# Performance work log

Hardware: AMD Instinct MI355X
Metric: run time of the kernel (lower is better)

The kernel has to match this reference:

```python
import jax, jax.numpy as jnp
import numpy as np

T, B, IN = 256, 64, 512
HIDDEN = [512, 512, 512]
DILATIONS = [1, 2, 4]


def _lstm_scan(x, W_ih, W_hh, b_ih, b_hh):
    """Run an LSTMCell over leading time axis of x: [Td, N, D] -> [Td, N, H]."""
    H = W_hh.shape[1]
    N = x.shape[1]
    h0 = jnp.zeros((N, H), x.dtype)
    c0 = jnp.zeros((N, H), x.dtype)

    def step(carry, xt):
        h, c = carry
        gates = xt @ W_ih.T + b_ih + h @ W_hh.T + b_hh  # [N, 4H], torch order i,f,g,o
        i, f, g, o = jnp.split(gates, 4, axis=-1)
        c = jax.nn.sigmoid(f) * c + jax.nn.sigmoid(i) * jnp.tanh(g)
        h = jax.nn.sigmoid(o) * jnp.tanh(c)
        return (h, c), h

    _, hs = jax.lax.scan(step, (h0, c0), x)
    return hs


def _drnn_layer(x, rate, W_ih, W_hh, b_ih, b_hh):
    """Dilated RNN layer. x: [T, B, D] with T % rate == 0.
    Torch code concats `rate` consecutive timesteps along batch -> one dilated step;
    reshape [T,B,D] -> [T//rate, rate*B, D] reproduces exactly that layout, and the
    chunk/unroll at the end is the inverse reshape."""
    Tn, Bn, D = x.shape
    Td = Tn // rate
    xd = x.reshape(Td, rate * Bn, D)
    hs = _lstm_scan(xd, W_ih, W_hh, b_ih, b_hh)  # [Td, rate*B, H]
    return hs.reshape(Tn, Bn, W_hh.shape[1])


def setup_inputs() -> dict:
    key = jax.random.key(0)
    ks = jax.random.split(key, 1 + 4 * len(HIDDEN))
    inp = {"x": jax.random.normal(ks[0], (T, B, IN), dtype=jnp.float32)}
    in_dim = IN
    ki = 1
    for li, H in enumerate(HIDDEN):
        bound = 1.0 / np.sqrt(H)
        inp[f"W_ih{li}"] = jax.random.uniform(ks[ki + 0], (4 * H, in_dim), jnp.float32, -bound, bound)
        inp[f"W_hh{li}"] = jax.random.uniform(ks[ki + 1], (4 * H, H), jnp.float32, -bound, bound)
        inp[f"b_ih{li}"] = jax.random.uniform(ks[ki + 2], (4 * H,), jnp.float32, -bound, bound)
        inp[f"b_hh{li}"] = jax.random.uniform(ks[ki + 3], (4 * H,), jnp.float32, -bound, bound)
        ki += 4
        in_dim = H
    return inp


def reference(x,
              W_ih0, W_hh0, b_ih0, b_hh0,
              W_ih1, W_hh1, b_ih1, b_hh1,
              W_ih2, W_hh2, b_ih2, b_hh2):
    params = [(W_ih0, W_hh0, b_ih0, b_hh0),
              (W_ih1, W_hh1, b_ih1, b_hh1),
              (W_ih2, W_hh2, b_ih2, b_hh2)]
    h = x
    for (Wih, Whh, bih, bhh), rate in zip(params, DILATIONS):
        h = _drnn_layer(h, rate, Wih, Whh, bih, bhh)
    return h  # [T, B, HIDDEN[-1]]
```

## Files before the change

kernel.cpp:

```cpp
#include <hip/hip_runtime.h>

typedef __attribute__((ext_vector_type(8))) short bf16x8;
typedef __attribute__((ext_vector_type(4))) float f32x4;

__device__ __forceinline__ unsigned short f2bf(float x) {
    unsigned u = __float_as_uint(x);
    u += 0x7FFFu + ((u >> 16) & 1u);
    return (unsigned short)(u >> 16);
}
__device__ __forceinline__ float sigm(float x) { return 1.0f / (1.0f + __expf(-x)); }
__device__ __forceinline__ float ftanh(float x) {
    float e = __expf(2.f * x);
    return 1.f - 2.f / (e + 1.f);
}

__device__ __forceinline__ void gld16(const unsigned short* g, unsigned short* l) {
    __builtin_amdgcn_global_load_lds((const __attribute__((address_space(1))) void*)g,
                                     (__attribute__((address_space(3))) void*)l, 16, 0, 0);
}

__device__ __forceinline__ unsigned cohload(const unsigned* p) {
    unsigned v;
    asm volatile("global_load_dword %0, %1, off sc0 sc1\n\ts_waitcnt vmcnt(0)"
                 : "=v"(v) : "v"(p) : "memory");
    return v;
}
__device__ __forceinline__ void cohstore(unsigned* p, unsigned v) {
    asm volatile("global_store_dword %0, %1, off sc0 sc1" :: "v"(p), "v"(v) : "memory");
}

__global__ __launch_bounds__(256) void k_conv_x(const float* __restrict__ x,
                                                unsigned short* __restrict__ Xp) {
    int i = blockIdx.x * 256 + threadIdx.x;
    int rb = i >> 10, kc = (i >> 6) & 15, ln = i & 63;
    int row = (rb << 4) + (ln & 15);
    int k   = (kc << 5) + ((ln >> 4) << 3);
    const float* s = x + (size_t)row * 512 + k;
    float4 v0 = *(const float4*)s, v1 = *(const float4*)(s + 4);
    unsigned short o[8] = {f2bf(v0.x), f2bf(v0.y), f2bf(v0.z), f2bf(v0.w),
                           f2bf(v1.x), f2bf(v1.y), f2bf(v1.z), f2bf(v1.w)};
    *(bf16x8*)(Xp + (size_t)i * 8) = *(bf16x8*)o;
}

__global__ __launch_bounds__(256) void k_conv_w(const float* __restrict__ Wih,
                                                const float* __restrict__ Whh,
                                                unsigned short* __restrict__ Wp) {
    int i = blockIdx.x * 256 + threadIdx.x;
    int wrb = i >> 11, kc = (i >> 6) & 31, ln = i & 63;
    int j = (wrb << 4) + (ln & 15);
    int k = (kc << 5) + ((ln >> 4) << 3);
    int srow = (j & 3) * 512 + (j >> 2);
    const float* s = (k < 512) ? (Wih + (size_t)srow * 512 + k)
                               : (Whh + (size_t)srow * 512 + (k - 512));
    float4 v0 = *(const float4*)s, v1 = *(const float4*)(s + 4);
    unsigned short o[8] = {f2bf(v0.x), f2bf(v0.y), f2bf(v0.z), f2bf(v0.w),
                           f2bf(v1.x), f2bf(v1.y), f2bf(v1.z), f2bf(v1.w)};
    *(bf16x8*)(Wp + (size_t)i * 8) = *(bf16x8*)o;
}

struct DP {
    const unsigned short* Xp;
    unsigned short *Hp0, *Hp1, *Hp2;
    const unsigned short *Wp0, *Wp1, *Wp2;
    const float *bi0, *bh0, *bi1, *bh1, *bi2, *bh2;
    float* Out;
    unsigned int* flags;
};

__device__ __forceinline__ void quadT(f32x4 a, int sq, float& G0, float& G1, float& G2, float& G3) {
    float a0 = a[0], a1 = a[1], a2 = a[2], a3 = a[3];
    float p1 = (sq & 1) ? a0 : a1; float g1_ = __shfl_xor(p1, 1);
    float p2 = (sq & 1) ? a2 : a3; float g2_ = __shfl_xor(p2, 1);
    float m0 = (sq & 1) ? g1_ : a0, m1 = (sq & 1) ? a1 : g1_;
    float m2 = (sq & 1) ? g2_ : a2, m3 = (sq & 1) ? a3 : g2_;
    float q1 = (sq & 2) ? m0 : m2; float h1_ = __shfl_xor(q1, 2);
    float q2 = (sq & 2) ? m1 : m3; float h2_ = __shfl_xor(q2, 2);
    G0 = (sq & 2) ? h1_ : m0; G1 = (sq & 2) ? h2_ : m1;
    G2 = (sq & 2) ? m2 : h1_; G3 = (sq & 2) ? m3 : h2_;
}

#define PIN8(A,B,C,D,E,F,G,H) \
    asm volatile("" : "+v"(A),"+v"(B),"+v"(C),"+v"(D),"+v"(E),"+v"(F),"+v"(G),"+v"(H))

__global__ __launch_bounds__(256, 1) void k_drnn(DP p) {
    const int tid = threadIdx.x, lane = tid & 63, wv = tid >> 6;
    const int l15 = lane & 15, lhi = lane >> 4, sq = l15 & 3;

    int b = blockIdx.x, l, c, w, T, P, N;
    if (b < 64)       { l = 0; c = b >> 5;         w = b & 31; T = 256; P = 1; N = 64; }
    else if (b < 128) { l = 1; c = (b >> 5) & 1;   w = b & 31; T = 128; P = 2; N = 128; }
    else              { l = 2; c = (b - 128) >> 5; w = b & 31; T = 64;  P = 2; N = 256; }
    const int cid = (l == 0) ? c : (l == 1 ? 2 + c : 4 + c);

    const unsigned short* Xs = (l == 0) ? p.Xp : (l == 1 ? p.Hp0 : p.Hp1);
    unsigned short*       Hd = (l == 0) ? p.Hp0 : (l == 1 ? p.Hp1 : p.Hp2);
    const unsigned short* Ws = (l == 0) ? p.Wp0 : (l == 1 ? p.Wp1 : p.Wp2);
    const float* bi = (l == 0) ? p.bi0 : (l == 1 ? p.bi1 : p.bi2);
    const float* bh = (l == 0) ? p.bh0 : (l == 1 ? p.bh1 : p.bh2);
    const int R0 = c * (P * 32);

    __shared__ unsigned short At[65536];

    const unsigned short* wbase = Ws + ((size_t)(((w << 2) + wv) * 32) << 9) + lane * 8;
#define DECLW(n) bf16x8 w##n = *(const bf16x8*)(wbase + (n << 9));
    DECLW(0) DECLW(1) DECLW(2) DECLW(3) DECLW(4) DECLW(5) DECLW(6) DECLW(7)
    DECLW(8) DECLW(9) DECLW(10) DECLW(11) DECLW(12) DECLW(13) DECLW(14) DECLW(15)
    DECLW(16) DECLW(17) DECLW(18) DECLW(19) DECLW(20) DECLW(21) DECLW(22) DECLW(23)
    DECLW(24) DECLW(25) DECLW(26) DECLW(27) DECLW(28) DECLW(29) DECLW(30) DECLW(31)

    const int hcol = (w << 4) + (wv << 2) + (l15 >> 2);
    const float bs0 = bi[hcol]        + bh[hcol];
    const float bs1 = bi[512 + hcol]  + bh[512 + hcol];
    const float bs2 = bi[1024 + hcol] + bh[1024 + hcol];
    const float bs3 = bi[1536 + hcol] + bh[1536 + hcol];

    const int kch = hcol >> 5;
    const int lane16 = (((hcol & 31) >> 3) << 4) + ((lhi << 2) + sq);
    const int st_lt = lane16 * 8 + (hcol & 7);

    float cst0 = 0.f, cst1 = 0.f, cst2 = 0.f, cst3 = 0.f;
    unsigned int* flags = p.flags;

#define KPn(na, nb) { \
    bf16x8 xa = *(const bf16x8*)(a0 + ((na) << 9)); \
    bf16x8 xb = *(const bf16x8*)(a1 + ((na) << 9)); \
    bf16x8 ya = *(const bf16x8*)(a0 + ((nb) << 9)); \
    bf16x8 yb = *(const bf16x8*)(a1 + ((nb) << 9)); \
    e0 = __builtin_amdgcn_mfma_f32_16x16x32_bf16(xa, w##na, e0, 0, 0, 0); \
    e1 = __builtin_amdgcn_mfma_f32_16x16x32_bf16(xb, w##na, e1, 0, 0, 0); \
    o0 = __builtin_amdgcn_mfma_f32_16x16x32_bf16(ya, w##nb, o0, 0, 0, 0); \
    o1 = __builtin_amdgcn_mfma_f32_16x16x32_bf16(yb, w##nb, o1, 0, 0, 0); }

#define PWST(RV, CSTV, PR) { \
    float G0, G1, G2, G3; quadT(RV, sq, G0, G1, G2, G3); \
    float cn = sigm(G1 + bs1) * CSTV + sigm(G0 + bs0) * ftanh(G2 + bs2); \
    float hn = sigm(G3 + bs3) * ftanh(cn); CSTV = cn; \
    const int Rw = RxB + (PR); \
    __hip_atomic_store(Hd + ((size_t)((Rw * 16 + kch) << 9) + st_lt), f2bf(hn), \
                       __ATOMIC_RELAXED, __HIP_MEMORY_SCOPE_AGENT); \
    if (l == 2) p.Out[((size_t)((Rw << 4) + (lhi << 2) + sq)) * 512 + hcol] = hn; }

#define DOPASS(PI, CA, CB) { \
    const unsigned short* a0 = At + (((PI) * 64) << 9) + lane * 8; \
    const unsigned short* a1 = a0 + (32 << 9); \
    f32x4 e0 = {0.f,0.f,0.f,0.f}, o0 = {0.f,0.f,0.f,0.f}; \
    f32x4 e1 = {0.f,0.f,0.f,0.f}, o1 = {0.f,0.f,0.f,0.f}; \
    KPn(0,1) KPn(2,3) KPn(4,5) KPn(6,7) KPn(8,9) KPn(10,11) KPn(12,13) KPn(14,15) \
    KPn(16,17) KPn(18,19) KPn(20,21) KPn(22,23) KPn(24,25) KPn(26,27) KPn(28,29) KPn(30,31) \
    f32x4 r0 = e0 + o0, r1 = e1 + o1; \
    PWST(r0, CA, (PI) * 2) PWST(r1, CB, (PI) * 2 + 1) }

    for (int t = 0; t < T; ++t) {
        PIN8(w0,w1,w2,w3,w4,w5,w6,w7);
        PIN8(w8,w9,w10,w11,w12,w13,w14,w15);
        PIN8(w16,w17,w18,w19,w20,w21,w22,w23);
        PIN8(w24,w25,w26,w27,w28,w29,w30,w31);

        const int RxB = (t * N + R0) >> 4;

        if (l == 0) {
            #pragma unroll
            for (int i = 0; i < 8; ++i) {
                int q = (wv << 3) + i, rb = q >> 4, kc = q & 15;
                gld16(Xs + ((size_t)((RxB + rb) * 16 + kc) << 9) + lane * 8,
                      &At[(rb * 32 + kc) << 9]);
            }
        }

        if (wv == 0 && t > 0) {
            const unsigned* fp = flags + cid * 32 + (lane & 31);
            const unsigned need = (unsigned)t;
            int n = 0;
            for (;;) {
                unsigned v = cohload(fp);
                if (__all((lane >= 32) || (v >= need))) break;
                if (++n > (1 << 20)) break;
            }
        }
        if (wv == 1 && l == 1) {
            const unsigned* fp = flags + lane;
            const unsigned need = (unsigned)(2 * t + 2);
            int n = 0;
            for (;;) {
                unsigned v = cohload(fp);
                if (__all(v >= need)) break;
                if (++n > (1 << 20)) break;
            }
        }
        if (wv == 1 && l == 2) {
            const unsigned* fp = flags + (2 + (c & 1)) * 32 + (lane & 31);
            const unsigned need = (unsigned)(2 * t + (c >> 1) + 1);
            int n = 0;
            for (;;) {
                unsigned v = cohload(fp);
                if (__all((lane >= 32) || (v >= need))) break;
                if (++n > (1 << 20)) break;
            }
        }
        __syncthreads();

        if (l == 0) {
            if (t > 0) {
                const int RhB = ((t - 1) * N + R0) >> 4;
                #pragma unroll
                for (int i = 0; i < 8; ++i) {
                    int q = (wv << 3) + i, rb = q >> 4, kc = q & 15;
                    gld16(Hd + ((size_t)((RhB + rb) * 16 + kc) << 9) + lane * 8,
                          &At[(rb * 32 + 16 + kc) << 9]);
                }
            } else {
                #pragma unroll
                for (int rb = 0; rb < 2; ++rb)
                    #pragma unroll
                    for (int it = 0; it < 4; ++it)
                        *(float4*)&At[((rb * 32 + 16) << 9) + (it * 256 + tid) * 8] =
                            (float4){0.f, 0.f, 0.f, 0.f};
            }
            __builtin_amdgcn_sched_barrier(0);

            const unsigned short* a0 = At + lane * 8;
            const unsigned short* a1 = a0 + (32 << 9);
            f32x4 e0 = {0.f,0.f,0.f,0.f}, o0 = {0.f,0.f,0.f,0.f};
            f32x4 e1 = {0.f,0.f,0.f,0.f}, o1 = {0.f,0.f,0.f,0.f};
            KPn(0,1) KPn(2,3) KPn(4,5) KPn(6,7)
            KPn(8,9) KPn(10,11) KPn(12,13) KPn(14,15)
            __syncthreads();
            KPn(16,17) KPn(18,19) KPn(20,21) KPn(22,23)
            KPn(24,25) KPn(26,27) KPn(28,29) KPn(30,31)
            f32x4 r0 = e0 + o0, r1 = e1 + o1;
            PWST(r0, cst0, 0) PWST(r1, cst1, 1)
        } else {
            #pragma unroll
            for (int i = 0; i < 16; ++i) {
                int q = (wv << 4) + i, rb = q >> 4, kc = q & 15;
                gld16(Xs + ((size_t)((RxB + rb) * 16 + kc) << 9) + lane * 8,
                      &At[(rb * 32 + kc) << 9]);
            }
            if (t > 0) {
                const int RhB = ((t - 1) * N + R0) >> 4;
                #pragma unroll
                for (int i = 0; i < 16; ++i) {
                    int q = (wv << 4) + i, rb = q >> 4, kc = q & 15;
                    gld16(Hd + ((size_t)((RhB + rb) * 16 + kc) << 9) + lane * 8,
                          &At[(rb * 32 + 16 + kc) << 9]);
                }
            } else {
                #pragma unroll
                for (int rb = 0; rb < 4; ++rb)
                    #pragma unroll
                    for (int it = 0; it < 4; ++it)
                        *(float4*)&At[((rb * 32 + 16) << 9) + (it * 256 + tid) * 8] =
                            (float4){0.f, 0.f, 0.f, 0.f};
            }
            __syncthreads();
            DOPASS(0, cst0, cst1)
            DOPASS(1, cst2, cst3)
        }

        asm volatile("s_waitcnt vmcnt(0)" ::: "memory");
        __syncthreads();
        if (tid == 0) cohstore(flags + cid * 32 + w, (unsigned)(t + 1));
    }
}

extern "C" void kernel_launch(void* const* d_in, const int* in_sizes, int n_in,
                              void* d_out, int out_size, void* d_ws, size_t ws_size,
                              hipStream_t stream)
{
    const float* x = (const float*)d_in[0];
    const float* Wih[3] = {(const float*)d_in[1], (const float*)d_in[5], (const float*)d_in[9]};
    const float* Whh[3] = {(const float*)d_in[2], (const float*)d_in[6], (const float*)d_in[10]};
    const float* bih[3] = {(const float*)d_in[3], (const float*)d_in[7], (const float*)d_in[11]};
    const float* bhh[3] = {(const float*)d_in[4], (const float*)d_in[8], (const float*)d_in[12]};

    char* wp = (char*)d_ws;
    const size_t SZ_A = (size_t)16384 * 512;
    unsigned short* Xp  = (unsigned short*)wp; wp += SZ_A * 2;
    unsigned short* Hp0 = (unsigned short*)wp; wp += SZ_A * 2;
    unsigned short* Hp1 = (unsigned short*)wp; wp += SZ_A * 2;
    unsigned short* Hp2 = (unsigned short*)wp; wp += SZ_A * 2;
    unsigned short* Wp[3];
    for (int l = 0; l < 3; ++l) { Wp[l] = (unsigned short*)wp; wp += (size_t)2048 * 1024 * 2; }
    unsigned int* flags = (unsigned int*)wp;

    hipMemsetAsync(flags, 0, 8 * 32 * sizeof(unsigned int), stream);
    k_conv_x<<<dim3(4096), dim3(256), 0, stream>>>(x, Xp);
    for (int l = 0; l < 3; ++l)
        k_conv_w<<<dim3(1024), dim3(256), 0, stream>>>(Wih[l], Whh[l], Wp[l]);

    DP dp;
    dp.Xp = Xp; dp.Hp0 = Hp0; dp.Hp1 = Hp1; dp.Hp2 = Hp2;
    dp.Wp0 = Wp[0]; dp.Wp1 = Wp[1]; dp.Wp2 = Wp[2];
    dp.bi0 = bih[0]; dp.bh0 = bhh[0];
    dp.bi1 = bih[1]; dp.bh1 = bhh[1];
    dp.bi2 = bih[2]; dp.bh2 = bhh[2];
    dp.Out = (float*)d_out; dp.flags = flags;

    k_drnn<<<dim3(256), dim3(256), 0, stream>>>(dp);
}
```

Before: 1.029 ms.

## Split intra-layer and cross-layer flags, write-through separate layer inputs, cheaper polling

The persistent wavefront kernel now keeps its recurrent hidden state in ordinary stores. It writes the next layer's input through a separate buffer with write-through (sc0 sc1) stores, and uses separate flag arrays for intra-layer and cross-layer dependencies. Intra-layer flag polling uses an L2-scope load and falls back to a system-coherent load after many spins. Blocks are interleaved across layers by blockIdx, and quad shuffles use DPP instead of ds_bpermute. The aim is to cut synchronization latency per time step, at the cost of added memory traffic and coherence assumptions about L2 visibility across XCDs.

```diff
diff --git a/kernel.cpp b/kernel.cpp
--- a/kernel.cpp
+++ b/kernel.cpp
@@ -19,14 +19,30 @@
                                      (__attribute__((address_space(3))) void*)l, 16, 0, 0);
 }
 
-__device__ __forceinline__ unsigned cohload(const unsigned* p) {
+__device__ __forceinline__ unsigned ld_l2(const unsigned* p) {
+    unsigned v;
+    asm volatile("global_load_dword %0, %1, off sc0\n\ts_waitcnt vmcnt(0)"
+                 : "=v"(v) : "v"(p) : "memory");
+    return v;
+}
+__device__ __forceinline__ unsigned ld_mall(const unsigned* p) {
     unsigned v;
     asm volatile("global_load_dword %0, %1, off sc0 sc1\n\ts_waitcnt vmcnt(0)"
                  : "=v"(v) : "v"(p) : "memory");
     return v;
 }
-__device__ __forceinline__ void cohstore(unsigned* p, unsigned v) {
+__device__ __forceinline__ void st_flag(unsigned* p, unsigned v) {
     asm volatile("global_store_dword %0, %1, off sc0 sc1" :: "v"(p), "v"(v) : "memory");
+}
+__device__ __forceinline__ void st_wt16(unsigned short* p, unsigned v) {
+    asm volatile("global_store_short %0, %1, off sc0 sc1" :: "v"(p), "v"(v) : "memory");
+}
+
+__device__ __forceinline__ float dppx1(float x) {
+    return __int_as_float(__builtin_amdgcn_mov_dpp(__float_as_int(x), 0xB1, 0xF, 0xF, true));
+}
+__device__ __forceinline__ float dppx2(float x) {
+    return __int_as_float(__builtin_amdgcn_mov_dpp(__float_as_int(x), 0x4E, 0xF, 0xF, true));
 }
 
 __global__ __launch_bounds__(256) void k_conv_x(const float* __restrict__ x,
@@ -61,6 +77,7 @@
 struct DP {
     const unsigned short* Xp;
     unsigned short *Hp0, *Hp1, *Hp2;
+    unsigned short *Xq1, *Xq2;
     const unsigned short *Wp0, *Wp1, *Wp2;
     const float *bi0, *bh0, *bi1, *bh1, *bi2, *bh2;
     float* Out;
@@ -69,12 +86,12 @@
 
 __device__ __forceinline__ void quadT(f32x4 a, int sq, float& G0, float& G1, float& G2, float& G3) {
     float a0 = a[0], a1 = a[1], a2 = a[2], a3 = a[3];
-    float p1 = (sq & 1) ? a0 : a1; float g1_ = __shfl_xor(p1, 1);
-    float p2 = (sq & 1) ? a2 : a3; float g2_ = __shfl_xor(p2, 1);
+    float p1 = (sq & 1) ? a0 : a1; float g1_ = dppx1(p1);
+    float p2 = (sq & 1) ? a2 : a3; float g2_ = dppx1(p2);
     float m0 = (sq & 1) ? g1_ : a0, m1 = (sq & 1) ? a1 : g1_;
     float m2 = (sq & 1) ? g2_ : a2, m3 = (sq & 1) ? a3 : g2_;
-    float q1 = (sq & 2) ? m0 : m2; float h1_ = __shfl_xor(q1, 2);
-    float q2 = (sq & 2) ? m1 : m3; float h2_ = __shfl_xor(q2, 2);
+    float q1 = (sq & 2) ? m0 : m2; float h1_ = dppx2(q1);
+    float q2 = (sq & 2) ? m1 : m3; float h2_ = dppx2(q2);
     G0 = (sq & 2) ? h1_ : m0; G1 = (sq & 2) ? h2_ : m1;
     G2 = (sq & 2) ? m2 : h1_; G3 = (sq & 2) ? m3 : h2_;
 }
@@ -86,14 +103,16 @@
     const int tid = threadIdx.x, lane = tid & 63, wv = tid >> 6;
     const int l15 = lane & 15, lhi = lane >> 4, sq = l15 & 3;
 
-    int b = blockIdx.x, l, c, w, T, P, N;
-    if (b < 64)       { l = 0; c = b >> 5;         w = b & 31; T = 256; P = 1; N = 64; }
-    else if (b < 128) { l = 1; c = (b >> 5) & 1;   w = b & 31; T = 128; P = 2; N = 128; }
-    else              { l = 2; c = (b - 128) >> 5; w = b & 31; T = 64;  P = 2; N = 256; }
-    const int cid = (l == 0) ? c : (l == 1 ? 2 + c : 4 + c);
-
-    const unsigned short* Xs = (l == 0) ? p.Xp : (l == 1 ? p.Hp0 : p.Hp1);
+    const int b = blockIdx.x;
+    const int cid = b & 7, w = b >> 3;
+    int l, c, T, P, N;
+    if (cid < 2)      { l = 0; c = cid;     T = 256; P = 1; N = 64;  }
+    else if (cid < 4) { l = 1; c = cid - 2; T = 128; P = 2; N = 128; }
+    else              { l = 2; c = cid - 4; T = 64;  P = 2; N = 256; }
+
+    const unsigned short* Xs = (l == 0) ? p.Xp  : (l == 1 ? p.Xq1 : p.Xq2);
     unsigned short*       Hd = (l == 0) ? p.Hp0 : (l == 1 ? p.Hp1 : p.Hp2);
+    unsigned short*       Xw = (l == 0) ? p.Xq1 : (l == 1 ? p.Xq2 : nullptr);
     const unsigned short* Ws = (l == 0) ? p.Wp0 : (l == 1 ? p.Wp1 : p.Wp2);
     const float* bi = (l == 0) ? p.bi0 : (l == 1 ? p.bi1 : p.bi2);
     const float* bh = (l == 0) ? p.bh0 : (l == 1 ? p.bh1 : p.bh2);
@@ -119,7 +138,9 @@
     const int st_lt = lane16 * 8 + (hcol & 7);
 
     float cst0 = 0.f, cst1 = 0.f, cst2 = 0.f, cst3 = 0.f;
-    unsigned int* flags = p.flags;
+    unsigned int* iflag = p.flags;
+    unsigned int* cflag = p.flags + 256;
+    int fastok = 1;
 
 #define KPn(na, nb) { \
     bf16x8 xa = *(const bf16x8*)(a0 + ((na) << 9)); \
@@ -131,16 +152,12 @@
     o0 = __builtin_amdgcn_mfma_f32_16x16x32_bf16(ya, w##nb, o0, 0, 0, 0); \
     o1 = __builtin_amdgcn_mfma_f32_16x16x32_bf16(yb, w##nb, o1, 0, 0, 0); }
 
-#define PWST(RV, CSTV, PR) { \
+#define PWC(RV, CSTV, HV) { \
     float G0, G1, G2, G3; quadT(RV, sq, G0, G1, G2, G3); \
     float cn = sigm(G1 + bs1) * CSTV + sigm(G0 + bs0) * ftanh(G2 + bs2); \
-    float hn = sigm(G3 + bs3) * ftanh(cn); CSTV = cn; \
-    const int Rw = RxB + (PR); \
-    __hip_atomic_store(Hd + ((size_t)((Rw * 16 + kch) << 9) + st_lt), f2bf(hn), \
-                       __ATOMIC_RELAXED, __HIP_MEMORY_SCOPE_AGENT); \
-    if (l == 2) p.Out[((size_t)((Rw << 4) + (lhi << 2) + sq)) * 512 + hcol] = hn; }
-
-#define DOPASS(PI, CA, CB) { \
+    HV = sigm(G3 + bs3) * ftanh(cn); CSTV = cn; }
+
+#define DOPASS(PI, CA, CB, HA, HB) { \
     const unsigned short* a0 = At + (((PI) * 64) << 9) + lane * 8; \
     const unsigned short* a1 = a0 + (32 << 9); \
     f32x4 e0 = {0.f,0.f,0.f,0.f}, o0 = {0.f,0.f,0.f,0.f}; \
@@ -148,7 +165,7 @@
     KPn(0,1) KPn(2,3) KPn(4,5) KPn(6,7) KPn(8,9) KPn(10,11) KPn(12,13) KPn(14,15) \
     KPn(16,17) KPn(18,19) KPn(20,21) KPn(22,23) KPn(24,25) KPn(26,27) KPn(28,29) KPn(30,31) \
     f32x4 r0 = e0 + o0, r1 = e1 + o1; \
-    PWST(r0, CA, (PI) * 2) PWST(r1, CB, (PI) * 2 + 1) }
+    PWC(r0, CA, HA) PWC(r1, CB, HB) }
 
     for (int t = 0; t < T; ++t) {
         PIN8(w0,w1,w2,w3,w4,w5,w6,w7);
@@ -168,37 +185,38 @@
         }
 
         if (wv == 0 && t > 0) {
-            const unsigned* fp = flags + cid * 32 + (lane & 31);
+            const unsigned* fp = iflag + cid * 32 + (lane & 31);
             const unsigned need = (unsigned)t;
             int n = 0;
             for (;;) {
-                unsigned v = cohload(fp);
+                unsigned v = fastok ? ld_l2(fp) : ld_mall(fp);
                 if (__all((lane >= 32) || (v >= need))) break;
-                if (++n > (1 << 20)) break;
+                if (fastok && ++n > 2048) fastok = 0;
             }
         }
         if (wv == 1 && l == 1) {
-            const unsigned* fp = flags + lane;
-            const unsigned need = (unsigned)(2 * t + 2);
+            const unsigned* fp = cflag + lane;
+            const unsigned need = (unsigned)(2 * t + (lane >> 5) + 1);
             int n = 0;
             for (;;) {
-                unsigned v = cohload(fp);
+                unsigned v = ld_mall(fp);
                 if (__all(v >= need)) break;
-                if (++n > (1 << 20)) break;
+                if (++n > (1 << 22)) break;
             }
         }
         if (wv == 1 && l == 2) {
-            const unsigned* fp = flags + (2 + (c & 1)) * 32 + (lane & 31);
+            const unsigned* fp = cflag + (2 + (c & 1)) * 32 + (lane & 31);
             const unsigned need = (unsigned)(2 * t + (c >> 1) + 1);
             int n = 0;
             for (;;) {
-                unsigned v = cohload(fp);
+                unsigned v = ld_mall(fp);
                 if (__all((lane >= 32) || (v >= need))) break;
-                if (++n > (1 << 20)) break;
+                if (++n > (1 << 22)) break;
             }
         }
         __syncthreads();
 
+        float hv0, hv1, hv2 = 0.f, hv3 = 0.f;
         if (l == 0) {
             if (t > 0) {
                 const int RhB = ((t - 1) * N + R0) >> 4;
@@ -228,7 +246,7 @@
             KPn(16,17) KPn(18,19) KPn(20,21) KPn(22,23)
             KPn(24,25) KPn(26,27) KPn(28,29) KPn(30,31)
             f32x4 r0 = e0 + o0, r1 = e1 + o1;
-            PWST(r0, cst0, 0) PWST(r1, cst1, 1)
+            PWC(r0, cst0, hv0) PWC(r1, cst1, hv1)
         } else {
             #pragma unroll
             for (int i = 0; i < 16; ++i) {
@@ -253,14 +271,45 @@
                             (float4){0.f, 0.f, 0.f, 0.f};
             }
             __syncthreads();
-            DOPASS(0, cst0, cst1)
-            DOPASS(1, cst2, cst3)
-        }
-
-        asm volatile("s_waitcnt vmcnt(0)" ::: "memory");
-        __syncthreads();
-        if (tid == 0) cohstore(flags + cid * 32 + w, (unsigned)(t + 1));
+            DOPASS(0, cst0, cst1, hv0, hv1)
+            DOPASS(1, cst2, cst3, hv2, hv3)
+        }
+
+        const unsigned short hb0 = f2bf(hv0), hb1 = f2bf(hv1);
+        const unsigned short hb2 = f2bf(hv2), hb3 = f2bf(hv3);
+        const size_t i0 = ((size_t)((RxB + 0) * 16 + kch) << 9) + st_lt;
+        const size_t i1 = ((size_t)((RxB + 1) * 16 + kch) << 9) + st_lt;
+        const size_t i2 = ((size_t)((RxB + 2) * 16 + kch) << 9) + st_lt;
+        const size_t i3 = ((size_t)((RxB + 3) * 16 + kch) << 9) + st_lt;
+        Hd[i0] = hb0; Hd[i1] = hb1;
+        if (P == 2) { Hd[i2] = hb2; Hd[i3] = hb3; }
+        if (l == 2) {
+            p.Out[((size_t)(((RxB + 0) << 4) + (lhi << 2) + sq)) * 512 + hcol] = hv0;
+            p.Out[((size_t)(((RxB + 1) << 4) + (lhi << 2) + sq)) * 512 + hcol] = hv1;
+            p.Out[((size_t)(((RxB + 2) << 4) + (lhi << 2) + sq)) * 512 + hcol] = hv2;
+            p.Out[((size_t)(((RxB + 3) << 4) + (lhi << 2) + sq)) * 512 + hcol] = hv3;
+        }
+        asm volatile("" ::: "memory");
+        __builtin_amdgcn_sched_barrier(0);
+        if (l == 0) { st_wt16(Xw + i0, hb0); st_wt16(Xw + i1, hb1); }
+        else if (l == 1) { st_wt16(Xw + i0, hb0); st_wt16(Xw + i1, hb1);
+                           st_wt16(Xw + i2, hb2); st_wt16(Xw + i3, hb3); }
+        __builtin_amdgcn_sched_barrier(0);
+        if (l == 0)      asm volatile("s_waitcnt vmcnt(2)" ::: "memory");
+        else if (l == 1) asm volatile("s_waitcnt vmcnt(4)" ::: "memory");
+        else             asm volatile("s_waitcnt vmcnt(0)" ::: "memory");
+        __builtin_amdgcn_sched_barrier(0);
+        __builtin_amdgcn_s_barrier();
+        __builtin_amdgcn_sched_barrier(0);
+        if (tid == 0) {
+            st_flag(iflag + cid * 32 + w, (unsigned)(t + 1));
+            if (l < 2 && t > 0) st_flag(cflag + cid * 32 + w, (unsigned)t);
+        }
     }
+
+    asm volatile("s_waitcnt vmcnt(0)" ::: "memory");
+    __builtin_amdgcn_s_barrier();
+    if (tid == 0 && l < 2) st_flag(cflag + cid * 32 + w, (unsigned)T);
 }
 
 extern "C" void kernel_launch(void* const* d_in, const int* in_sizes, int n_in,
@@ -275,21 +324,26 @@
 
     char* wp = (char*)d_ws;
     const size_t SZ_A = (size_t)16384 * 512;
+    unsigned int* flags = (unsigned int*)wp; wp += 4096;
     unsigned short* Xp  = (unsigned short*)wp; wp += SZ_A * 2;
     unsigned short* Hp0 = (unsigned short*)wp; wp += SZ_A * 2;
     unsigned short* Hp1 = (unsigned short*)wp; wp += SZ_A * 2;
     unsigned short* Hp2 = (unsigned short*)wp; wp += SZ_A * 2;
     unsigned short* Wp[3];
     for (int l = 0; l < 3; ++l) { Wp[l] = (unsigned short*)wp; wp += (size_t)2048 * 1024 * 2; }
-    unsigned int* flags = (unsigned int*)wp;
-
-    hipMemsetAsync(flags, 0, 8 * 32 * sizeof(unsigned int), stream);
+    unsigned short* Xq1 = (unsigned short*)wp; wp += SZ_A * 2;
+    unsigned short* Xq2 = (unsigned short*)wp; wp += SZ_A * 2;
+    const size_t need = (size_t)(wp - (char*)d_ws);
+    if (ws_size < need) { Xq1 = Hp0; Xq2 = Hp1; }
+
+    hipMemsetAsync(flags, 0, 4096, stream);
     k_conv_x<<<dim3(4096), dim3(256), 0, stream>>>(x, Xp);
     for (int l = 0; l < 3; ++l)
         k_conv_w<<<dim3(1024), dim3(256), 0, stream>>>(Wih[l], Whh[l], Wp[l]);
 
     DP dp;
     dp.Xp = Xp; dp.Hp0 = Hp0; dp.Hp1 = Hp1; dp.Hp2 = Hp2;
+    dp.Xq1 = Xq1; dp.Xq2 = Xq2;
     dp.Wp0 = Wp[0]; dp.Wp1 = Wp[1]; dp.Wp2 = Wp[2];
     dp.bi0 = bih[0]; dp.bh0 = bhh[0];
     dp.bi1 = bih[1]; dp.bh1 = bhh[1];
```

New measurement: 1.293 ms. 25.7% more time.
